# Performance work log

Measured on AMD Instinct MI355X. Metric: run time of the kernel, lower is better.

The kernel has to match this reference:

```python
import jax, jax.numpy as jnp
import numpy as np

N_NODES = 100000
N_EDGES = 1600000
IN_FEATS = 128
N_HIDDEN = 128
N_CLASSES = 16


def setup_inputs() -> dict:
    key = jax.random.key(0)
    ks = jax.random.split(key, 10)
    features = jax.random.normal(ks[0], (N_NODES, IN_FEATS), dtype=jnp.float32)
    src = jax.random.randint(ks[1], (N_EDGES,), 0, N_NODES, dtype=jnp.int32)
    dst = jax.random.randint(ks[2], (N_EDGES,), 0, N_NODES, dtype=jnp.int32)
    # Glorot-ish init for the three GraphConv layers
    def glorot(k, fan_in, fan_out):
        s = (2.0 / (fan_in + fan_out)) ** 0.5
        return jax.random.normal(k, (fan_in, fan_out), dtype=jnp.float32) * s
    W0 = glorot(ks[3], IN_FEATS, N_HIDDEN)
    b0 = jnp.zeros((N_HIDDEN,), jnp.float32)
    W1 = glorot(ks[4], N_HIDDEN, N_HIDDEN)
    b1 = jnp.zeros((N_HIDDEN,), jnp.float32)
    W2 = glorot(ks[5], N_HIDDEN, N_CLASSES)
    b2 = jnp.zeros((N_CLASSES,), jnp.float32)
    return {"features": features, "src": src, "dst": dst,
            "W0": W0, "b0": b0, "W1": W1, "b1": b1, "W2": W2, "b2": b2}


def _graph_conv(h, src, dst, src_norm, dst_norm, W, b, act):
    # DGL GraphConv, norm='both':
    # out = D_dst^{-1/2} * sum_{(u->v) in E} (D_src^{-1/2} h)_u W  + b
    h = h * src_norm[:, None]           # [N, F] scale by out-degree^-1/2
    hw = h @ W                          # [N, F_out] transform before gather (F_out <= F here)
    agg = jax.ops.segment_sum(hw[src], dst, num_segments=h.shape[0])  # scatter-add over edges
    out = agg * dst_norm[:, None] + b
    return act(out)


def reference(features, src, dst, W0, b0, W1, b1, W2, b2):
    N = features.shape[0]
    ones = jnp.ones(src.shape[0], dtype=jnp.float32)
    out_deg = jnp.clip(jax.ops.segment_sum(ones, src, num_segments=N), 1.0)
    in_deg = jnp.clip(jax.ops.segment_sum(ones, dst, num_segments=N), 1.0)
    src_norm = out_deg ** -0.5
    dst_norm = in_deg ** -0.5

    relu = jax.nn.relu
    pos_sigmoid = lambda x: jax.nn.sigmoid(x) + 1e-8

    h = features.astype(jnp.float32)
    h = _graph_conv(h, src, dst, src_norm, dst_norm, W0, b0, relu)
    h = _graph_conv(h, src, dst, src_norm, dst_norm, W1, b1, relu)
    h = _graph_conv(h, src, dst, src_norm, dst_norm, W2, b2, pos_sigmoid)
    return h
```

## Files before the change

kernel.cpp:

```cpp
#include <hip/hip_runtime.h>
#include <hip/hip_bf16.h>


constexpr int BLK = 256;
constexpr int CH = 8192;

typedef __attribute__((ext_vector_type(8))) short s8v;
typedef __attribute__((ext_vector_type(4))) float f4v;

__device__ __forceinline__ float bflo(unsigned int u) { return __uint_as_float(u << 16); }
__device__ __forceinline__ float bfhi(unsigned int u) { return __uint_as_float(u & 0xffff0000u); }
__device__ __forceinline__ unsigned int bfr(float f) {
    unsigned int u = __float_as_uint(f);
    return (u + 0x7fffu + ((u >> 16) & 1u)) >> 16;
}
__device__ __forceinline__ unsigned int bfpack(float lo, float hi) {
    unsigned int ul = __float_as_uint(lo), uh = __float_as_uint(hi);
    unsigned int rl = (ul + 0x7fffu + ((ul >> 16) & 1u)) >> 16;
    unsigned int rh = (uh + 0x7fffu + ((uh >> 16) & 1u)) & 0xffff0000u;
    return rl | rh;
}

__global__ __launch_bounds__(256) void k_pcount(const int* __restrict__ src, const int* __restrict__ dst,
                                                int* __restrict__ pmat_d, int* __restrict__ pmat_s,
                                                int E, int NB) {
    __shared__ int hd[1024], hs[1024];
    for (int i = threadIdx.x; i < 1024; i += 256) { hd[i] = 0; hs[i] = 0; }
    __syncthreads();
    int b = blockIdx.x;
    int e0 = b * CH, e1 = min(e0 + CH, E);
    for (int e = e0 + threadIdx.x; e < e1; e += 256) {
        atomicAdd(&hd[dst[e] >> 7], 1);
        atomicAdd(&hs[src[e] >> 7], 1);
    }
    __syncthreads();
    for (int i = threadIdx.x; i < NB; i += 256) {
        pmat_d[(size_t)b * NB + i] = hd[i];
        pmat_s[(size_t)b * NB + i] = hs[i];
    }
}

__global__ __launch_bounds__(1024) void k_pscan(const int* __restrict__ pmat_d, const int* __restrict__ pmat_s,
                                                int* __restrict__ bbase_d, int* __restrict__ bbase_s,
                                                int* __restrict__ omat_d, int* __restrict__ omat_s,
                                                unsigned short* __restrict__ B2pad, unsigned short* __restrict__ HW16pad,
                                                int N, int NB, int nblk) {
    const int* pmat = blockIdx.x ? pmat_s : pmat_d;
    int* bbase = blockIdx.x ? bbase_s : bbase_d;
    int* omat  = blockIdx.x ? omat_s : omat_d;
    __shared__ int s[1024];
    int t = threadIdx.x;
    int tot = 0;
    if (t < NB) {
#pragma unroll 8
        for (int b = 0; b < nblk; b++) tot += pmat[(size_t)b * NB + t];
    }
    s[t] = (t < NB) ? tot : 0;
    __syncthreads();
    for (int d = 1; d < 1024; d <<= 1) {
        int x = (t >= d) ? s[t - d] : 0;
        __syncthreads();
        s[t] += x;
        __syncthreads();
    }
    if (t < NB) {
        int base = s[t] - tot;
        bbase[t] = base;
        if (t == NB - 1) bbase[NB] = s[t];
        int run = base;
#pragma unroll 8
        for (int b = 0; b < nblk; b++) {
            size_t idx = (size_t)b * NB + t;
            omat[idx] = run;
            run += pmat[idx];
        }
    }
    if (blockIdx.x == 1) {
        if (t < 128) B2pad[(size_t)N * 128 + t] = 0;
        if (t < 16)  HW16pad[(size_t)N * 16 + t] = 0;
    }
}

__global__ __launch_bounds__(256) void k_pscatter(const int* __restrict__ src, const int* __restrict__ dst,
                                                  const int* __restrict__ omat_d, const int* __restrict__ omat_s,
                                                  unsigned int* __restrict__ ebuf_d, unsigned char* __restrict__ ebuf_s,
                                                  int E, int NB) {
    __shared__ int cd[1024], cs[1024];
    int b = blockIdx.x;
    for (int i = threadIdx.x; i < NB; i += 256) {
        cd[i] = omat_d[(size_t)b * NB + i];
        cs[i] = omat_s[(size_t)b * NB + i];
    }
    __syncthreads();
    int e0 = b * CH, e1 = min(e0 + CH, E);
    for (int e = e0 + threadIdx.x; e < e1; e += 256) {
        int s_ = src[e], d_ = dst[e];
        int pd = atomicAdd(&cd[d_ >> 7], 1);
        ebuf_d[pd] = (unsigned)s_ | ((unsigned)(d_ & 127) << 17);
        int ps = atomicAdd(&cs[s_ >> 7], 1);
        ebuf_s[ps] = (unsigned char)(s_ & 127);
    }
}

__global__ __launch_bounds__(256) void k_build(const unsigned int* __restrict__ ebuf_d,
                                               const int* __restrict__ bbase_d,
                                               const unsigned char* __restrict__ ebuf_s,
                                               const int* __restrict__ bbase_s,
                                               int* __restrict__ csr, int* __restrict__ rowptr,
                                               int* __restrict__ deg, float* __restrict__ srcn,
                                               const float* __restrict__ W0, const float* __restrict__ W1,
                                               const float* __restrict__ W2,
                                               unsigned short* __restrict__ Wt0, unsigned short* __restrict__ Wt1,
                                               unsigned short* __restrict__ Wt2,
                                               int N, int NB) {
    int b = blockIdx.x, tx = threadIdx.x;
    if (b < NB) {
        __shared__ unsigned int rec[3584];
        __shared__ unsigned int sorted[4096];
        __shared__ int cnt[128];
        __shared__ int pws[129];
        __shared__ int wcur[128];
        int k = b;
        int ebeg = bbase_d[k];
        int ecnt = bbase_d[k + 1] - ebeg;
        if (ecnt > 3584) ecnt = 3584;
        int pbase = ((ebeg + 3) & ~3) + k * 512;
        if (tx < 128) cnt[tx] = 0;
        __syncthreads();
        for (int i = tx; i < ecnt; i += 256) {
            unsigned int r = ebuf_d[ebeg + i];
            rec[i] = r;
            atomicAdd(&cnt[(r >> 17) & 127], 1);
        }
        __syncthreads();
        int pc = (tx < 128) ? ((cnt[tx] + 3) & ~3) : 0;
        if (tx < 128) wcur[tx] = pc;
        __syncthreads();
        for (int d = 1; d < 128; d <<= 1) {
            int x = (tx < 128 && tx >= d) ? wcur[tx - d] : 0;
            __syncthreads();
            if (tx < 128) wcur[tx] += x;
            __syncthreads();
        }
        if (tx < 128) pws[tx] = wcur[tx] - pc;
        if (tx == 127) pws[128] = wcur[127];
        __syncthreads();
        int pecnt = pws[128];
        for (int i = tx; i < pecnt; i += 256) sorted[i] = (unsigned)N;
        if (tx < 128) wcur[tx] = pws[tx];
        __syncthreads();
        for (int i = tx; i < ecnt; i += 256) {
            unsigned int r = rec[i];
            int p = atomicAdd(&wcur[(r >> 17) & 127], 1);
            sorted[p] = r & 0x1FFFFu;
        }
        __syncthreads();
        for (int i = tx; i < pecnt; i += 256) csr[pbase + i] = (int)sorted[i];
        if (tx < 128) {
            int v = k * 128 + tx;
            if (v < N) { rowptr[v] = pbase + pws[tx]; deg[v] = cnt[tx]; }
        }
    } else if (b < 2 * NB) {
        __shared__ int scnt[128];
        int k = b - NB;
        if (tx < 128) scnt[tx] = 0;
        __syncthreads();
        int beg = bbase_s[k], end = bbase_s[k + 1];
        for (int i = beg + tx; i < end; i += 256) atomicAdd(&scnt[ebuf_s[i]], 1);
        __syncthreads();
        if (tx < 128) {
            int v = k * 128 + tx;
            if (v < N) {
                int c = scnt[tx];
                if (c < 1) c = 1;
                srcn[v] = rsqrtf((float)c);
            }
        }
    } else {
        int bb = b - 2 * NB;
        const float* W; unsigned short* Wt; int total, base;
        if (bb < 64)      { W = W0; Wt = Wt0; total = 16384; base = bb * 256; }
        else if (bb < 128){ W = W1; Wt = Wt1; total = 16384; base = (bb - 64) * 256; }
        else              { W = W2; Wt = Wt2; total = 2048;  base = (bb - 128) * 256; }
        int i = base + tx;
        if (i < total) {
            int Ncol = total >> 7;
            int c = i >> 7, kk = i & 127;
            Wt[i] = (unsigned short)bfr(W[kk * Ncol + c]);
        }
    }
}

template <int NT, int F32IN>
__global__ __launch_bounds__(256, 2) void k_gemm_mfma(const unsigned short* __restrict__ Ab,
                                                      const float* __restrict__ Af,
                                                      const float* __restrict__ srcn,
                                                      const unsigned short* __restrict__ Wt,
                                                      unsigned short* __restrict__ outb, int M) {
    int tx = threadIdx.x;
    int w = tx >> 6, l = tx & 63;
    int lr = l & 15, lg = l >> 4;
    int wbase = (blockIdx.x * 4 + w) * 64;

    s8v bf[NT][4];
#pragma unroll
    for (int nt = 0; nt < NT; ++nt) {
        int br = nt * 16 + lr;
#pragma unroll
        for (int kk = 0; kk < 4; ++kk)
            bf[nt][kk] = *(const s8v*)(Wt + (size_t)br * 128 + (kk * 4 + lg) * 8);
    }

    union U { uint4 u; s8v v; };
    U bufA[4], bufB[4];

#define LOADA(S, DST)                                                          \
    {                                                                          \
        int r0_ = wbase + (S) * 16 + lr;                                       \
        if (r0_ < M) {                                                         \
            if (F32IN) {                                                       \
                float sn_ = srcn[r0_];                                         \
                _Pragma("unroll")                                              \
                for (int kk = 0; kk < 4; ++kk) {                               \
                    const float4* pf = (const float4*)(Af + (size_t)r0_ * 128 + (kk * 4 + lg) * 8); \
                    float4 x = pf[0], y = pf[1];                               \
                    DST[kk].u.x = bfpack(x.x * sn_, x.y * sn_);                \
                    DST[kk].u.y = bfpack(x.z * sn_, x.w * sn_);                \
                    DST[kk].u.z = bfpack(y.x * sn_, y.y * sn_);                \
                    DST[kk].u.w = bfpack(y.z * sn_, y.w * sn_);                \
                }                                                              \
            } else {                                                           \
                _Pragma("unroll")                                              \
                for (int kk = 0; kk < 4; ++kk)                                 \
                    DST[kk].u = *(const uint4*)(Ab + (size_t)r0_ * 128 + (kk * 4 + lg) * 8); \
            }                                                                  \
        } else {                                                               \
            _Pragma("unroll")                                                  \
            for (int kk = 0; kk < 4; ++kk) DST[kk].u = make_uint4(0u, 0u, 0u, 0u); \
        }                                                                      \
    }

#define COMPUTE(S, CUR)                                                        \
    {                                                                          \
        f4v acc[NT];                                                           \
        _Pragma("unroll")                                                      \
        for (int nt = 0; nt < NT; ++nt) { acc[nt][0] = 0.f; acc[nt][1] = 0.f; acc[nt][2] = 0.f; acc[nt][3] = 0.f; } \
        _Pragma("unroll")                                                      \
        for (int kk = 0; kk < 4; ++kk) {                                       \
            _Pragma("unroll")                                                  \
            for (int nt = 0; nt < NT; ++nt)                                    \
                acc[nt] = __builtin_amdgcn_mfma_f32_16x16x32_bf16(CUR[kk].v, bf[nt][kk], acc[nt], 0, 0, 0); \
        }                                                                      \
        _Pragma("unroll")                                                      \
        for (int nt = 0; nt < NT; ++nt) {                                      \
            _Pragma("unroll")                                                  \
            for (int i = 0; i < 4; ++i) {                                      \
                int R = wbase + (S) * 16 + lg * 4 + i;                         \
                if (R < M) outb[(size_t)R * (NT * 16) + nt * 16 + lr] = (unsigned short)bfr(acc[nt][i]); \
            }                                                                  \
        }                                                                      \
    }

    LOADA(0, bufA)
    LOADA(1, bufB)
    COMPUTE(0, bufA)
    LOADA(2, bufA)
    COMPUTE(1, bufB)
    LOADA(3, bufB)
    COMPUTE(2, bufA)
    COMPUTE(3, bufB)
#undef LOADA
#undef COMPUTE
}

__global__ __launch_bounds__(256) void k_aggN(const unsigned short* __restrict__ hw,
                                              const int* __restrict__ csr,
                                              const int* __restrict__ rowptr,
                                              const int* __restrict__ deg,
                                              const float* __restrict__ srcn,
                                              const float* __restrict__ bias,
                                              unsigned short* __restrict__ out, int N) {
    int t = blockIdx.x * 256 + threadIdx.x;
    int v = t >> 4, sub = t & 15;
    if (v >= N) return;
    int s0 = rowptr[v];
    int dg = deg[v];
    int plen = (dg + 3) & ~3;
    const unsigned short* hws = hw + sub * 8;

    float a0 = 0.f, a1 = 0.f, a2 = 0.f, a3 = 0.f, a4 = 0.f, a5 = 0.f, a6 = 0.f, a7 = 0.f;
#define ACC8(V)                                                         \
    a0 += bflo(V.x); a1 += bfhi(V.x); a2 += bflo(V.y); a3 += bfhi(V.y); \
    a4 += bflo(V.z); a5 += bfhi(V.z); a6 += bflo(V.w); a7 += bfhi(V.w);
    int e = s0;
    int end8 = s0 + (plen & ~7);
    for (; e < end8; e += 8) {
        int4 xa = *(const int4*)(csr + e);
        int4 xb = *(const int4*)(csr + e + 4);
        uint4 v0 = *(const uint4*)(hws + (size_t)xa.x * 128);
        uint4 v1 = *(const uint4*)(hws + (size_t)xa.y * 128);
        uint4 v2 = *(const uint4*)(hws + (size_t)xa.z * 128);
        uint4 v3 = *(const uint4*)(hws + (size_t)xa.w * 128);
        uint4 v4 = *(const uint4*)(hws + (size_t)xb.x * 128);
        uint4 v5 = *(const uint4*)(hws + (size_t)xb.y * 128);
        uint4 v6 = *(const uint4*)(hws + (size_t)xb.z * 128);
        uint4 v7 = *(const uint4*)(hws + (size_t)xb.w * 128);
        ACC8(v0) ACC8(v1) ACC8(v2) ACC8(v3) ACC8(v4) ACC8(v5) ACC8(v6) ACC8(v7)
    }
    if (plen & 4) {
        int4 xs = *(const int4*)(csr + e);
        uint4 v0 = *(const uint4*)(hws + (size_t)xs.x * 128);
        uint4 v1 = *(const uint4*)(hws + (size_t)xs.y * 128);
        uint4 v2 = *(const uint4*)(hws + (size_t)xs.z * 128);
        uint4 v3 = *(const uint4*)(hws + (size_t)xs.w * 128);
        ACC8(v0) ACC8(v1) ACC8(v2) ACC8(v3)
    }
#undef ACC8
    int d = dg < 1 ? 1 : dg;
    float dn = rsqrtf((float)d);
    float4 b0 = *(const float4*)(bias + sub * 8);
    float4 b1 = *(const float4*)(bias + sub * 8 + 4);
    float sn = srcn[v];
    float o0 = fmaxf(a0 * dn + b0.x, 0.f) * sn, o1 = fmaxf(a1 * dn + b0.y, 0.f) * sn;
    float o2 = fmaxf(a2 * dn + b0.z, 0.f) * sn, o3 = fmaxf(a3 * dn + b0.w, 0.f) * sn;
    float o4 = fmaxf(a4 * dn + b1.x, 0.f) * sn, o5 = fmaxf(a5 * dn + b1.y, 0.f) * sn;
    float o6 = fmaxf(a6 * dn + b1.z, 0.f) * sn, o7 = fmaxf(a7 * dn + b1.w, 0.f) * sn;
    uint4 o;
    o.x = bfpack(o0, o1); o.y = bfpack(o2, o3);
    o.z = bfpack(o4, o5); o.w = bfpack(o6, o7);
    *(uint4*)(out + (size_t)v * 128 + sub * 8) = o;
}

__global__ __launch_bounds__(256) void k_agg16(const unsigned short* __restrict__ hw,
                                               const int* __restrict__ csr,
                                               const int* __restrict__ rowptr,
                                               const int* __restrict__ deg,
                                               const float* __restrict__ bias,
                                               float* __restrict__ out, int N) {
    int t = blockIdx.x * 256 + threadIdx.x;
    int v = t >> 2, q = t & 3;
    if (v >= N) return;
    int s0 = rowptr[v];
    int dg = deg[v];
    int plen = (dg + 3) & ~3;
    const unsigned short* hws = hw + q * 4;
    float a0 = 0.f, a1 = 0.f, a2 = 0.f, a3 = 0.f;
#define ACC4(V)                                                         \
    a0 += bflo(V.x); a1 += bfhi(V.x); a2 += bflo(V.y); a3 += bfhi(V.y);
    for (int e = s0; e < s0 + plen; e += 4) {
        int4 xs = *(const int4*)(csr + e);
        uint2 v0 = *(const uint2*)(hws + (size_t)xs.x * 16);
        uint2 v1 = *(const uint2*)(hws + (size_t)xs.y * 16);
        uint2 v2 = *(const uint2*)(hws + (size_t)xs.z * 16);
        uint2 v3 = *(const uint2*)(hws + (size_t)xs.w * 16);
        ACC4(v0) ACC4(v1) ACC4(v2) ACC4(v3)
    }
#undef ACC4
    int d = dg < 1 ? 1 : dg;
    float dn = rsqrtf((float)d);
    float4 b = *(const float4*)(bias + q * 4);
    float o0 = 1.f / (1.f + __expf(-(a0 * dn + b.x))) + 1e-8f;
    float o1 = 1.f / (1.f + __expf(-(a1 * dn + b.y))) + 1e-8f;
    float o2 = 1.f / (1.f + __expf(-(a2 * dn + b.z))) + 1e-8f;
    float o3 = 1.f / (1.f + __expf(-(a3 * dn + b.w))) + 1e-8f;
    *(float4*)(out + (size_t)v * 16 + q * 4) = make_float4(o0, o1, o2, o3);
}

extern "C" void kernel_launch(void* const* d_in, const int* in_sizes, int n_in,
                              void* d_out, int out_size, void* d_ws, size_t ws_size,
                              hipStream_t stream) {
    const float* features = (const float*)d_in[0];
    const int*   src      = (const int*)d_in[1];
    const int*   dst      = (const int*)d_in[2];
    const float* W0       = (const float*)d_in[3];
    const float* b0       = (const float*)d_in[4];
    const float* W1       = (const float*)d_in[5];
    const float* b1       = (const float*)d_in[6];
    const float* W2       = (const float*)d_in[7];
    const float* b2       = (const float*)d_in[8];
    float* out = (float*)d_out;

    const int N = in_sizes[0] / 128;
    const int E = in_sizes[1];
    const int NB = (N + 127) >> 7;
    const int nblk = (E + CH - 1) / CH;

    char* ws = (char*)d_ws;
    size_t off = 0;
    auto alloc = [&](size_t bytes) -> char* {
        char* p = ws + off;
        off += (bytes + 255) / 256 * 256;
        return p;
    };
    int* pmat_d  = (int*)alloc((size_t)nblk * NB * 4);
    int* pmat_s  = (int*)alloc((size_t)nblk * NB * 4);
    int* omat_d  = (int*)alloc((size_t)nblk * NB * 4);
    int* omat_s  = (int*)alloc((size_t)nblk * NB * 4);
    int* bbase_d = (int*)alloc((size_t)(NB + 1) * 4);
    int* bbase_s = (int*)alloc((size_t)(NB + 1) * 4);
    unsigned int*  ebuf_d = (unsigned int*)alloc((size_t)E * 4);
    unsigned char* ebuf_s = (unsigned char*)alloc((size_t)E);
    int* csr     = (int*)alloc(((size_t)E + (size_t)NB * 512 + 512) * 4);
    int* rowptr  = (int*)alloc((size_t)(N + 1) * 4);
    int* deg     = (int*)alloc((size_t)N * 4);
    float* srcn  = (float*)alloc((size_t)N * 4);
    unsigned short* Wt0 = (unsigned short*)alloc(128 * 128 * 2);
    unsigned short* Wt1 = (unsigned short*)alloc(128 * 128 * 2);
    unsigned short* Wt2 = (unsigned short*)alloc(16 * 128 * 2);
    unsigned short* B1 = (unsigned short*)alloc((size_t)N * 128 * 2);
    unsigned short* B2 = (unsigned short*)alloc((size_t)(N + 1) * 128 * 2);
    unsigned short* HW16 = (unsigned short*)alloc((size_t)(N + 1) * 16 * 2);
    (void)ws_size; (void)n_in; (void)out_size;

    k_pcount<<<nblk, 256, 0, stream>>>(src, dst, pmat_d, pmat_s, E, NB);
    k_pscan<<<2, 1024, 0, stream>>>(pmat_d, pmat_s, bbase_d, bbase_s, omat_d, omat_s, B2, HW16, N, NB, nblk);
    k_pscatter<<<nblk, 256, 0, stream>>>(src, dst, omat_d, omat_s, ebuf_d, ebuf_s, E, NB);
    k_build<<<2 * NB + 136, 256, 0, stream>>>(ebuf_d, bbase_d, ebuf_s, bbase_s, csr, rowptr, deg, srcn,
                                              W0, W1, W2, Wt0, Wt1, Wt2, N, NB);

    int gb = (N + 255) / 256;
    int anb = (N * 16 + 255) / 256;
    int a16b = (N * 4 + 255) / 256;

    k_gemm_mfma<8, 1><<<gb, 256, 0, stream>>>(nullptr, features, srcn, Wt0, B2, N);
    k_aggN<<<anb, 256, 0, stream>>>(B2, csr, rowptr, deg, srcn, b0, B1, N);
    k_gemm_mfma<8, 0><<<gb, 256, 0, stream>>>(B1, nullptr, nullptr, Wt1, B2, N);
    k_aggN<<<anb, 256, 0, stream>>>(B2, csr, rowptr, deg, srcn, b1, B1, N);
    k_gemm_mfma<1, 0><<<gb, 256, 0, stream>>>(B1, nullptr, nullptr, Wt2, HW16, N);
    k_agg16<<<a16b, 256, 0, stream>>>(HW16, csr, rowptr, deg, b2, out, N);
}
```

Baseline: 357.5 us.

## Overlap first GEMM with edge counting; fuse final GEMM into second aggregation

The first-layer GEMM no longer waits for the degree/CSR build. Its blocks share one launch with the edge-histogram blocks, it converts W0 to bf16 in registers, and the source-norm scaling moves into the layer-0 aggregation as a per-edge srcn multiply. The layer-1 aggregation now also applies the 128x16 W2 projection, using shared-memory weights and a wave shuffle reduction, which removes the separate small GEMM launch and its read of B1. The cost is a gather of srcn on every edge in layer 0 and heavy per-block W0 loading and conversion in the GEMM blocks.

New measurement: 388.8 us. 8.7% more time.

```diff
diff --git a/kernel.cpp b/kernel.cpp
--- a/kernel.cpp
+++ b/kernel.cpp
@@ -21,29 +21,109 @@
     return rl | rh;
 }
 
-__global__ __launch_bounds__(256) void k_pcount(const int* __restrict__ src, const int* __restrict__ dst,
-                                                int* __restrict__ pmat_d, int* __restrict__ pmat_s,
-                                                int E, int NB) {
+__global__ __launch_bounds__(256, 2) void k_mix1(const float* __restrict__ Af,
+                                                 const float* __restrict__ W0,
+                                                 unsigned short* __restrict__ outb, int M,
+                                                 const int* __restrict__ src, const int* __restrict__ dst,
+                                                 int* __restrict__ pmat_d, int* __restrict__ pmat_s,
+                                                 int E, int NB, int GB) {
     __shared__ int hd[1024], hs[1024];
-    for (int i = threadIdx.x; i < 1024; i += 256) { hd[i] = 0; hs[i] = 0; }
-    __syncthreads();
     int b = blockIdx.x;
-    int e0 = b * CH, e1 = min(e0 + CH, E);
-    for (int e = e0 + threadIdx.x; e < e1; e += 256) {
-        atomicAdd(&hd[dst[e] >> 7], 1);
-        atomicAdd(&hs[src[e] >> 7], 1);
-    }
-    __syncthreads();
-    for (int i = threadIdx.x; i < NB; i += 256) {
-        pmat_d[(size_t)b * NB + i] = hd[i];
-        pmat_s[(size_t)b * NB + i] = hs[i];
-    }
+    if (b >= GB) {
+        int bb = b - GB;
+        for (int i = threadIdx.x; i < 1024; i += 256) { hd[i] = 0; hs[i] = 0; }
+        __syncthreads();
+        int e0 = bb * CH, e1 = min(e0 + CH, E);
+        for (int e = e0 + threadIdx.x; e < e1; e += 256) {
+            atomicAdd(&hd[dst[e] >> 7], 1);
+            atomicAdd(&hs[src[e] >> 7], 1);
+        }
+        __syncthreads();
+        for (int i = threadIdx.x; i < NB; i += 256) {
+            pmat_d[(size_t)bb * NB + i] = hd[i];
+            pmat_s[(size_t)bb * NB + i] = hs[i];
+        }
+        return;
+    }
+    int tx = threadIdx.x;
+    int w = tx >> 6, l = tx & 63;
+    int lr = l & 15, lg = l >> 4;
+    int wbase = (b * 4 + w) * 64;
+
+    s8v bf[8][4];
+#pragma unroll
+    for (int nt = 0; nt < 8; ++nt) {
+        int c = nt * 16 + lr;
+#pragma unroll
+        for (int kk = 0; kk < 4; ++kk) {
+            s8v t;
+#pragma unroll
+            for (int j = 0; j < 8; ++j)
+                t[j] = (short)bfr(W0[(size_t)((kk * 4 + lg) * 8 + j) * 128 + c]);
+            bf[nt][kk] = t;
+        }
+    }
+
+    union U { uint4 u; s8v v; };
+    U bufA[4], bufB[4];
+
+#define LOADA0(S, DST)                                                         \
+    {                                                                          \
+        int r0_ = wbase + (S) * 16 + lr;                                       \
+        if (r0_ < M) {                                                         \
+            _Pragma("unroll")                                                  \
+            for (int kk = 0; kk < 4; ++kk) {                                   \
+                const float4* pf = (const float4*)(Af + (size_t)r0_ * 128 + (kk * 4 + lg) * 8); \
+                float4 x = pf[0], y = pf[1];                                   \
+                DST[kk].u.x = bfpack(x.x, x.y);                                \
+                DST[kk].u.y = bfpack(x.z, x.w);                                \
+                DST[kk].u.z = bfpack(y.x, y.y);                                \
+                DST[kk].u.w = bfpack(y.z, y.w);                                \
+            }                                                                  \
+        } else {                                                               \
+            _Pragma("unroll")                                                  \
+            for (int kk = 0; kk < 4; ++kk) DST[kk].u = make_uint4(0u, 0u, 0u, 0u); \
+        }                                                                      \
+    }
+
+#define COMPUTE0(S, CUR)                                                       \
+    {                                                                          \
+        f4v acc[8];                                                            \
+        _Pragma("unroll")                                                      \
+        for (int nt = 0; nt < 8; ++nt) { acc[nt][0] = 0.f; acc[nt][1] = 0.f; acc[nt][2] = 0.f; acc[nt][3] = 0.f; } \
+        _Pragma("unroll")                                                      \
+        for (int kk = 0; kk < 4; ++kk) {                                       \
+            _Pragma("unroll")                                                  \
+            for (int nt = 0; nt < 8; ++nt)                                     \
+                acc[nt] = __builtin_amdgcn_mfma_f32_16x16x32_bf16(CUR[kk].v, bf[nt][kk], acc[nt], 0, 0, 0); \
+        }                                                                      \
+        _Pragma("unroll")                                                      \
+        for (int nt = 0; nt < 8; ++nt) {                                       \
+            _Pragma("unroll")                                                  \
+            for (int i = 0; i < 4; ++i) {                                      \
+                int R = wbase + (S) * 16 + lg * 4 + i;                         \
+                if (R < M) outb[(size_t)R * 128 + nt * 16 + lr] = (unsigned short)bfr(acc[nt][i]); \
+            }                                                                  \
+        }                                                                      \
+    }
+
+    LOADA0(0, bufA)
+    LOADA0(1, bufB)
+    COMPUTE0(0, bufA)
+    LOADA0(2, bufA)
+    COMPUTE0(1, bufB)
+    LOADA0(3, bufB)
+    COMPUTE0(2, bufA)
+    COMPUTE0(3, bufB)
+#undef LOADA0
+#undef COMPUTE0
 }
 
 __global__ __launch_bounds__(1024) void k_pscan(const int* __restrict__ pmat_d, const int* __restrict__ pmat_s,
                                                 int* __restrict__ bbase_d, int* __restrict__ bbase_s,
                                                 int* __restrict__ omat_d, int* __restrict__ omat_s,
                                                 unsigned short* __restrict__ B2pad, unsigned short* __restrict__ HW16pad,
+                                                float* __restrict__ srcnPad,
                                                 int N, int NB, int nblk) {
     const int* pmat = blockIdx.x ? pmat_s : pmat_d;
     int* bbase = blockIdx.x ? bbase_s : bbase_d;
@@ -78,6 +158,7 @@
     if (blockIdx.x == 1) {
         if (t < 128) B2pad[(size_t)N * 128 + t] = 0;
         if (t < 16)  HW16pad[(size_t)N * 16 + t] = 0;
+        if (t == 0)  srcnPad[N] = 0.f;
     }
 }
 
@@ -108,10 +189,8 @@
                                                const int* __restrict__ bbase_s,
                                                int* __restrict__ csr, int* __restrict__ rowptr,
                                                int* __restrict__ deg, float* __restrict__ srcn,
-                                               const float* __restrict__ W0, const float* __restrict__ W1,
-                                               const float* __restrict__ W2,
-                                               unsigned short* __restrict__ Wt0, unsigned short* __restrict__ Wt1,
-                                               unsigned short* __restrict__ Wt2,
+                                               const float* __restrict__ W1, const float* __restrict__ W2,
+                                               unsigned short* __restrict__ Wt1, unsigned short* __restrict__ Wt2,
                                                int N, int NB) {
     int b = blockIdx.x, tx = threadIdx.x;
     if (b < NB) {
@@ -179,9 +258,8 @@
     } else {
         int bb = b - 2 * NB;
         const float* W; unsigned short* Wt; int total, base;
-        if (bb < 64)      { W = W0; Wt = Wt0; total = 16384; base = bb * 256; }
-        else if (bb < 128){ W = W1; Wt = Wt1; total = 16384; base = (bb - 64) * 256; }
-        else              { W = W2; Wt = Wt2; total = 2048;  base = (bb - 128) * 256; }
+        if (bb < 64) { W = W1; Wt = Wt1; total = 16384; base = bb * 256; }
+        else         { W = W2; Wt = Wt2; total = 2048;  base = (bb - 64) * 256; }
         int i = base + tx;
         if (i < total) {
             int Ncol = total >> 7;
@@ -191,20 +269,17 @@
     }
 }
 
-template <int NT, int F32IN>
-__global__ __launch_bounds__(256, 2) void k_gemm_mfma(const unsigned short* __restrict__ Ab,
-                                                      const float* __restrict__ Af,
-                                                      const float* __restrict__ srcn,
-                                                      const unsigned short* __restrict__ Wt,
-                                                      unsigned short* __restrict__ outb, int M) {
+__global__ __launch_bounds__(256, 2) void k_gemmB(const unsigned short* __restrict__ Ab,
+                                                  const unsigned short* __restrict__ Wt,
+                                                  unsigned short* __restrict__ outb, int M) {
     int tx = threadIdx.x;
     int w = tx >> 6, l = tx & 63;
     int lr = l & 15, lg = l >> 4;
     int wbase = (blockIdx.x * 4 + w) * 64;
 
-    s8v bf[NT][4];
-#pragma unroll
-    for (int nt = 0; nt < NT; ++nt) {
+    s8v bf[8][4];
+#pragma unroll
+    for (int nt = 0; nt < 8; ++nt) {
         int br = nt * 16 + lr;
 #pragma unroll
         for (int kk = 0; kk < 4; ++kk)
@@ -218,22 +293,9 @@
     {                                                                          \
         int r0_ = wbase + (S) * 16 + lr;                                       \
         if (r0_ < M) {                                                         \
-            if (F32IN) {                                                       \
-                float sn_ = srcn[r0_];                                         \
-                _Pragma("unroll")                                              \
-                for (int kk = 0; kk < 4; ++kk) {                               \
-                    const float4* pf = (const float4*)(Af + (size_t)r0_ * 128 + (kk * 4 + lg) * 8); \
-                    float4 x = pf[0], y = pf[1];                               \
-                    DST[kk].u.x = bfpack(x.x * sn_, x.y * sn_);                \
-                    DST[kk].u.y = bfpack(x.z * sn_, x.w * sn_);                \
-                    DST[kk].u.z = bfpack(y.x * sn_, y.y * sn_);                \
-                    DST[kk].u.w = bfpack(y.z * sn_, y.w * sn_);                \
-                }                                                              \
-            } else {                                                           \
-                _Pragma("unroll")                                              \
-                for (int kk = 0; kk < 4; ++kk)                                 \
-                    DST[kk].u = *(const uint4*)(Ab + (size_t)r0_ * 128 + (kk * 4 + lg) * 8); \
-            }                                                                  \
+            _Pragma("unroll")                                                  \
+            for (int kk = 0; kk < 4; ++kk)                                     \
+                DST[kk].u = *(const uint4*)(Ab + (size_t)r0_ * 128 + (kk * 4 + lg) * 8); \
         } else {                                                               \
             _Pragma("unroll")                                                  \
             for (int kk = 0; kk < 4; ++kk) DST[kk].u = make_uint4(0u, 0u, 0u, 0u); \
@@ -242,21 +304,21 @@
 
 #define COMPUTE(S, CUR)                                                        \
     {                                                                          \
-        f4v acc[NT];                                                           \
+        f4v acc[8];                                                            \
         _Pragma("unroll")                                                      \
-        for (int nt = 0; nt < NT; ++nt) { acc[nt][0] = 0.f; acc[nt][1] = 0.f; acc[nt][2] = 0.f; acc[nt][3] = 0.f; } \
+        for (int nt = 0; nt < 8; ++nt) { acc[nt][0] = 0.f; acc[nt][1] = 0.f; acc[nt][2] = 0.f; acc[nt][3] = 0.f; } \
         _Pragma("unroll")                                                      \
         for (int kk = 0; kk < 4; ++kk) {                                       \
             _Pragma("unroll")                                                  \
-            for (int nt = 0; nt < NT; ++nt)                                    \
+            for (int nt = 0; nt < 8; ++nt)                                     \
                 acc[nt] = __builtin_amdgcn_mfma_f32_16x16x32_bf16(CUR[kk].v, bf[nt][kk], acc[nt], 0, 0, 0); \
         }                                                                      \
         _Pragma("unroll")                                                      \
-        for (int nt = 0; nt < NT; ++nt) {                                      \
+        for (int nt = 0; nt < 8; ++nt) {                                       \
             _Pragma("unroll")                                                  \
             for (int i = 0; i < 4; ++i) {                                      \
                 int R = wbase + (S) * 16 + lg * 4 + i;                         \
-                if (R < M) outb[(size_t)R * (NT * 16) + nt * 16 + lr] = (unsigned short)bfr(acc[nt][i]); \
+                if (R < M) outb[(size_t)R * 128 + nt * 16 + lr] = (unsigned short)bfr(acc[nt][i]); \
             }                                                                  \
         }                                                                      \
     }
@@ -289,33 +351,21 @@
     const unsigned short* hws = hw + sub * 8;
 
     float a0 = 0.f, a1 = 0.f, a2 = 0.f, a3 = 0.f, a4 = 0.f, a5 = 0.f, a6 = 0.f, a7 = 0.f;
-#define ACC8(V)                                                         \
-    a0 += bflo(V.x); a1 += bfhi(V.x); a2 += bflo(V.y); a3 += bfhi(V.y); \
-    a4 += bflo(V.z); a5 += bfhi(V.z); a6 += bflo(V.w); a7 += bfhi(V.w);
-    int e = s0;
-    int end8 = s0 + (plen & ~7);
-    for (; e < end8; e += 8) {
-        int4 xa = *(const int4*)(csr + e);
-        int4 xb = *(const int4*)(csr + e + 4);
-        uint4 v0 = *(const uint4*)(hws + (size_t)xa.x * 128);
-        uint4 v1 = *(const uint4*)(hws + (size_t)xa.y * 128);
-        uint4 v2 = *(const uint4*)(hws + (size_t)xa.z * 128);
-        uint4 v3 = *(const uint4*)(hws + (size_t)xa.w * 128);
-        uint4 v4 = *(const uint4*)(hws + (size_t)xb.x * 128);
-        uint4 v5 = *(const uint4*)(hws + (size_t)xb.y * 128);
-        uint4 v6 = *(const uint4*)(hws + (size_t)xb.z * 128);
-        uint4 v7 = *(const uint4*)(hws + (size_t)xb.w * 128);
-        ACC8(v0) ACC8(v1) ACC8(v2) ACC8(v3) ACC8(v4) ACC8(v5) ACC8(v6) ACC8(v7)
-    }
-    if (plen & 4) {
+#define ACC8S(V, S)                                                            \
+    a0 = fmaf(bflo(V.x), S, a0); a1 = fmaf(bfhi(V.x), S, a1);                  \
+    a2 = fmaf(bflo(V.y), S, a2); a3 = fmaf(bfhi(V.y), S, a3);                  \
+    a4 = fmaf(bflo(V.z), S, a4); a5 = fmaf(bfhi(V.z), S, a5);                  \
+    a6 = fmaf(bflo(V.w), S, a6); a7 = fmaf(bfhi(V.w), S, a7);
+    for (int e = s0; e < s0 + plen; e += 4) {
         int4 xs = *(const int4*)(csr + e);
+        float sa = srcn[xs.x], sb = srcn[xs.y], sc = srcn[xs.z], sd = srcn[xs.w];
         uint4 v0 = *(const uint4*)(hws + (size_t)xs.x * 128);
         uint4 v1 = *(const uint4*)(hws + (size_t)xs.y * 128);
         uint4 v2 = *(const uint4*)(hws + (size_t)xs.z * 128);
         uint4 v3 = *(const uint4*)(hws + (size_t)xs.w * 128);
-        ACC8(v0) ACC8(v1) ACC8(v2) ACC8(v3)
-    }
-#undef ACC8
+        ACC8S(v0, sa) ACC8S(v1, sb) ACC8S(v2, sc) ACC8S(v3, sd)
+    }
+#undef ACC8S
     int d = dg < 1 ? 1 : dg;
     float dn = rsqrtf((float)d);
     float4 b0 = *(const float4*)(bias + sub * 8);
@@ -329,6 +379,72 @@
     o.x = bfpack(o0, o1); o.y = bfpack(o2, o3);
     o.z = bfpack(o4, o5); o.w = bfpack(o6, o7);
     *(uint4*)(out + (size_t)v * 128 + sub * 8) = o;
+}
+
+__global__ __launch_bounds__(256) void k_aggF(const unsigned short* __restrict__ hw,
+                                              const int* __restrict__ csr,
+                                              const int* __restrict__ rowptr,
+                                              const int* __restrict__ deg,
+                                              const float* __restrict__ srcn,
+                                              const float* __restrict__ bias,
+                                              const unsigned short* __restrict__ Wt2,
+                                              unsigned short* __restrict__ hw16, int N) {
+    __shared__ unsigned short w2[2048];
+    ((uint4*)w2)[threadIdx.x] = ((const uint4*)Wt2)[threadIdx.x];
+    __syncthreads();
+    int t = blockIdx.x * 256 + threadIdx.x;
+    int v = t >> 4, sub = t & 15;
+    if (v >= N) return;
+    int s0 = rowptr[v];
+    int dg = deg[v];
+    int plen = (dg + 3) & ~3;
+    const unsigned short* hws = hw + sub * 8;
+
+    float a0 = 0.f, a1 = 0.f, a2 = 0.f, a3 = 0.f, a4 = 0.f, a5 = 0.f, a6 = 0.f, a7 = 0.f;
+#define ACC8(V)                                                         \
+    a0 += bflo(V.x); a1 += bfhi(V.x); a2 += bflo(V.y); a3 += bfhi(V.y); \
+    a4 += bflo(V.z); a5 += bfhi(V.z); a6 += bflo(V.w); a7 += bfhi(V.w);
+    for (int e = s0; e < s0 + plen; e += 4) {
+        int4 xs = *(const int4*)(csr + e);
+        uint4 v0 = *(const uint4*)(hws + (size_t)xs.x * 128);
+        uint4 v1 = *(const uint4*)(hws + (size_t)xs.y * 128);
+        uint4 v2 = *(const uint4*)(hws + (size_t)xs.z * 128);
+        uint4 v3 = *(const uint4*)(hws + (size_t)xs.w * 128);
+        ACC8(v0) ACC8(v1) ACC8(v2) ACC8(v3)
+    }
+#undef ACC8
+    int d = dg < 1 ? 1 : dg;
+    float dn = rsqrtf((float)d);
+    float4 b0 = *(const float4*)(bias + sub * 8);
+    float4 b1 = *(const float4*)(bias + sub * 8 + 4);
+    float sn = srcn[v];
+    float o0 = fmaxf(a0 * dn + b0.x, 0.f) * sn, o1 = fmaxf(a1 * dn + b0.y, 0.f) * sn;
+    float o2 = fmaxf(a2 * dn + b0.z, 0.f) * sn, o3 = fmaxf(a3 * dn + b0.w, 0.f) * sn;
+    float o4 = fmaxf(a4 * dn + b1.x, 0.f) * sn, o5 = fmaxf(a5 * dn + b1.y, 0.f) * sn;
+    float o6 = fmaxf(a6 * dn + b1.z, 0.f) * sn, o7 = fmaxf(a7 * dn + b1.w, 0.f) * sn;
+
+    float p[16];
+#pragma unroll
+    for (int c = 0; c < 16; ++c) {
+        uint4 wv = *(const uint4*)(w2 + c * 128 + sub * 8);
+        float s = 0.f;
+        s = fmaf(bflo(wv.x), o0, s); s = fmaf(bfhi(wv.x), o1, s);
+        s = fmaf(bflo(wv.y), o2, s); s = fmaf(bfhi(wv.y), o3, s);
+        s = fmaf(bflo(wv.z), o4, s); s = fmaf(bfhi(wv.z), o5, s);
+        s = fmaf(bflo(wv.w), o6, s); s = fmaf(bfhi(wv.w), o7, s);
+        p[c] = s;
+    }
+    float outv = 0.f;
+#pragma unroll
+    for (int c = 0; c < 16; ++c) {
+        float tt = p[c];
+        tt += __shfl_xor(tt, 1, 64);
+        tt += __shfl_xor(tt, 2, 64);
+        tt += __shfl_xor(tt, 4, 64);
+        tt += __shfl_xor(tt, 8, 64);
+        if (sub == c) outv = tt;
+    }
+    hw16[(size_t)v * 16 + sub] = (unsigned short)bfr(outv);
 }
 
 __global__ __launch_bounds__(256) void k_agg16(const unsigned short* __restrict__ hw,
@@ -403,8 +519,7 @@
     int* csr     = (int*)alloc(((size_t)E + (size_t)NB * 512 + 512) * 4);
     int* rowptr  = (int*)alloc((size_t)(N + 1) * 4);
     int* deg     = (int*)alloc((size_t)N * 4);
-    float* srcn  = (float*)alloc((size_t)N * 4);
-    unsigned short* Wt0 = (unsigned short*)alloc(128 * 128 * 2);
+    float* srcn  = (float*)alloc((size_t)(N + 1) * 4);
     unsigned short* Wt1 = (unsigned short*)alloc(128 * 128 * 2);
     unsigned short* Wt2 = (unsigned short*)alloc(16 * 128 * 2);
     unsigned short* B1 = (unsigned short*)alloc((size_t)N * 128 * 2);
@@ -412,20 +527,18 @@
     unsigned short* HW16 = (unsigned short*)alloc((size_t)(N + 1) * 16 * 2);
     (void)ws_size; (void)n_in; (void)out_size;
 
-    k_pcount<<<nblk, 256, 0, stream>>>(src, dst, pmat_d, pmat_s, E, NB);
-    k_pscan<<<2, 1024, 0, stream>>>(pmat_d, pmat_s, bbase_d, bbase_s, omat_d, omat_s, B2, HW16, N, NB, nblk);
-    k_pscatter<<<nblk, 256, 0, stream>>>(src, dst, omat_d, omat_s, ebuf_d, ebuf_s, E, NB);
-    k_build<<<2 * NB + 136, 256, 0, stream>>>(ebuf_d, bbase_d, ebuf_s, bbase_s, csr, rowptr, deg, srcn,
-                                              W0, W1, W2, Wt0, Wt1, Wt2, N, NB);
-
     int gb = (N + 255) / 256;
     int anb = (N * 16 + 255) / 256;
     int a16b = (N * 4 + 255) / 256;
 
-    k_gemm_mfma<8, 1><<<gb, 256, 0, stream>>>(nullptr, features, srcn, Wt0, B2, N);
+    k_mix1<<<gb + nblk, 256, 0, stream>>>(features, W0, B2, N, src, dst, pmat_d, pmat_s, E, NB, gb);
+    k_pscan<<<2, 1024, 0, stream>>>(pmat_d, pmat_s, bbase_d, bbase_s, omat_d, omat_s, B2, HW16, srcn, N, NB, nblk);
+    k_pscatter<<<nblk, 256, 0, stream>>>(src, dst, omat_d, omat_s, ebuf_d, ebuf_s, E, NB);
+    k_build<<<2 * NB + 72, 256, 0, stream>>>(ebuf_d, bbase_d, ebuf_s, bbase_s, csr, rowptr, deg, srcn,
+                                             W1, W2, Wt1, Wt2, N, NB);
+
     k_aggN<<<anb, 256, 0, stream>>>(B2, csr, rowptr, deg, srcn, b0, B1, N);
-    k_gemm_mfma<8, 0><<<gb, 256, 0, stream>>>(B1, nullptr, nullptr, Wt1, B2, N);
-    k_aggN<<<anb, 256, 0, stream>>>(B2, csr, rowptr, deg, srcn, b1, B1, N);
-    k_gemm_mfma<1, 0><<<gb, 256, 0, stream>>>(B1, nullptr, nullptr, Wt2, HW16, N);
+    k_gemmB<<<gb, 256, 0, stream>>>(B1, Wt1, B2, N);
+    k_aggF<<<anb, 256, 0, stream>>>(B2, csr, rowptr, deg, srcn, b1, Wt2, HW16, N);
     k_agg16<<<a16b, 256, 0, stream>>>(HW16, csr, rowptr, deg, b2, out, N);
 }
```
